# Optimization experiments

Measured on AMD Instinct MI355X. Metric: run time of the kernel, lower is better.

## Reference

```python
import jax, jax.numpy as jnp
import numpy as np

B, N, K = 2, 8192, 9
FEAT_C, COST_C, FLOW_C = 128, 64, 3
CH = [128, 128]          # PointConv output channels
MLP = [128, 64]          # pointwise Conv1d channels
WN = 16                  # WeightNet output width
HID = [8, 8]             # WeightNet hidden widths
SLOPE = 0.1              # leaky relu slope
EPS = 1e-5
CLAMP = (-200.0, 200.0)


def setup_inputs() -> dict:
    key = jax.random.key(0)
    ks = iter(jax.random.split(key, 64))
    def nrm(shape, s=0.02):
        return jax.random.normal(next(ks), shape, jnp.float32) * s
    inp = {}
    inp["xyz"] = jax.random.normal(next(ks), (B, N, 3), jnp.float32)
    inp["feats"] = jax.random.normal(next(ks), (B, FEAT_C, N), jnp.float32)
    inp["cost_volume"] = jax.random.normal(next(ks), (B, COST_C, N), jnp.float32)
    inp["flow"] = jax.random.normal(next(ks), (B, FLOW_C, N), jnp.float32)
    last = FEAT_C + COST_C + FLOW_C
    for i, co in enumerate(CH):
        cin = last + 3
        p = f"pc{i}_"
        inp[p + "w1"] = nrm((HID[0], 3)); inp[p + "b1"] = jnp.zeros((HID[0],), jnp.float32)
        inp[p + "w2"] = nrm((HID[1], HID[0])); inp[p + "b2"] = jnp.zeros((HID[1],), jnp.float32)
        inp[p + "w3"] = nrm((WN, HID[1])); inp[p + "b3"] = jnp.zeros((WN,), jnp.float32)
        inp[p + "linW"] = nrm((co, cin * WN)); inp[p + "linb"] = jnp.zeros((co,), jnp.float32)
        last = co
    for i, co in enumerate(MLP):
        inp[f"mlp{i}_W"] = nrm((co, last)); inp[f"mlp{i}_b"] = jnp.zeros((co,), jnp.float32)
        last = co
    inp["fc_W"] = nrm((3, last)); inp["fc_b"] = jnp.zeros((3,), jnp.float32)
    return inp


def _bn(x, axes):
    m = x.mean(axes, keepdims=True)
    v = x.var(axes, keepdims=True)
    return (x - m) / jnp.sqrt(v + EPS)


def _leaky(x):
    return jnp.where(x >= 0, x, SLOPE * x)


def _knn_idx(xyz, k):
    # xyz: [B,N,3] -> idx [B,N,K] of k nearest (incl. self)
    sq = jnp.sum(xyz * xyz, -1)                       # [B,N]
    d = sq[:, :, None] + sq[:, None, :] - 2.0 * jnp.einsum('bnc,bmc->bnm', xyz, xyz)
    return jax.lax.top_k(-d, k)[1]                    # [B,N,K]


def _gather(a, idx):
    # a: [B,N,C], idx: [B,N,K] -> [B,N,K,C]
    return jax.vmap(lambda x, i: x[i])(a, idx)


def _pointconv(xyz, points, idx, w1, b1, w2, b2, w3, b3, linW, linb):
    # xyz [B,N,3], points [B,C,N] -> [B,out,N]
    g_xyz = _gather(xyz, idx) - xyz[:, :, None, :]    # [B,N,K,3] relative coords
    g_pts = _gather(jnp.transpose(points, (0, 2, 1)), idx)  # [B,N,K,C]
    grouped = jnp.concatenate([g_pts, g_xyz], -1)     # [B,N,K,C+3]
    # WeightNet on relative coords: 3 -> 8 -> 8 -> 16 (bn+relu each)
    h = jax.nn.relu(_bn(g_xyz @ w1.T + b1, (0, 1, 2)))
    h = jax.nn.relu(_bn(h @ w2.T + b2, (0, 1, 2)))
    w = jax.nn.relu(_bn(h @ w3.T + b3, (0, 1, 2)))    # [B,N,K,WN]
    bsz, n = grouped.shape[0], grouped.shape[1]
    agg = jnp.einsum('bnkc,bnkw->bncw', grouped, w).reshape(bsz, n, -1)
    out = agg @ linW.T + linb                         # [B,N,out]
    out = _leaky(_bn(out, (0, 1)))
    return jnp.transpose(out, (0, 2, 1))              # [B,out,N]


def reference(xyz, feats, cost_volume, flow,
              pc0_w1, pc0_b1, pc0_w2, pc0_b2, pc0_w3, pc0_b3, pc0_linW, pc0_linb,
              pc1_w1, pc1_b1, pc1_w2, pc1_b2, pc1_w3, pc1_b3, pc1_linW, pc1_linb,
              mlp0_W, mlp0_b, mlp1_W, mlp1_b, fc_W, fc_b):
    idx = _knn_idx(xyz, K)
    x = jnp.concatenate([feats, cost_volume, flow], axis=1)  # [B, feat+cost+flow, N]
    x = _pointconv(xyz, x, idx, pc0_w1, pc0_b1, pc0_w2, pc0_b2, pc0_w3, pc0_b3, pc0_linW, pc0_linb)
    x = _pointconv(xyz, x, idx, pc1_w1, pc1_b1, pc1_w2, pc1_b2, pc1_w3, pc1_b3, pc1_linW, pc1_linb)
    x = _leaky(jnp.einsum('oc,bcn->bon', mlp0_W, x) + mlp0_b[None, :, None])
    x = _leaky(jnp.einsum('oc,bcn->bon', mlp1_W, x) + mlp1_b[None, :, None])
    fl = jnp.einsum('oc,bcn->bon', fc_W, x) + fc_b[None, :, None]
    return x, jnp.clip(fl, CLAMP[0], CLAMP[1])
```

## Files before the change

### kernel.cpp

```cpp
#include <hip/hip_runtime.h>

#define NBATCH 2
#define NPTS   8192
#define NPT    (NBATCH*NPTS)
#define KNN    9
#define SEG    16
#define SEGN   (NPTS/SEG)
#define SCAP   16
#define SSTR   17

typedef unsigned short u16;
typedef unsigned int   u32;
typedef short bf16x8 __attribute__((ext_vector_type(8)));
typedef float f32x4  __attribute__((ext_vector_type(4)));

__device__ __forceinline__ float wred(float v){
#pragma unroll
  for(int o=32;o>0;o>>=1) v += __shfl_down(v,o);
  return v;
}

__device__ __forceinline__ u16 f2b(float f){
  u32 u = __float_as_uint(f);
  return (u16)((u + 0x7fffu + ((u>>16)&1u)) >> 16);
}

__device__ __forceinline__ float bumpup(float x){
  u32 u = __float_as_uint(x);
  if(u == 0x80000000u) u = 1u;
  else if((int)u >= 0) u += 1u;
  else u -= 1u;
  return __uint_as_float(u);
}

__global__ __launch_bounds__(256) void k_build_xin(
    const float* __restrict__ feats, const float* __restrict__ cost,
    const float* __restrict__ flow, float* __restrict__ xin)
{
  __shared__ float buf[196][67];
  int t = threadIdx.x;
  int pt0 = blockIdx.x*64;
  int b = pt0 >> 13, n0 = pt0 & (NPTS-1);
  int lane = t & 63, grp = t >> 6;
  const float* f  = feats + (size_t)b*128*NPTS + n0 + lane;
  const float* cv = cost  + (size_t)b*64 *NPTS + n0 + lane;
  const float* fl = flow  + (size_t)b*3  *NPTS + n0 + lane;
  for(int c=grp; c<128; c+=4) buf[c][lane]      = f[(size_t)c*NPTS];
  for(int c=grp; c<64;  c+=4) buf[128+c][lane]  = cv[(size_t)c*NPTS];
  if(grp<3) buf[192+grp][lane] = fl[(size_t)grp*NPTS];
  else      buf[195][lane] = 0.f;
  __syncthreads();
  for(int e=t; e<64*49; e+=256){
    int p = e/49, q = e-p*49;
    float4 v = make_float4(buf[4*q][p], buf[4*q+1][p], buf[4*q+2][p], buf[4*q+3][p]);
    *(float4*)(xin + (size_t)(pt0+p)*196 + 4*q) = v;
  }
}

__global__ __launch_bounds__(256) void k_xyzs(
    const float* __restrict__ xyz, float4* __restrict__ xs)
{
  int pt = blockIdx.x*256 + threadIdx.x;
  int b = pt >> 13, n = pt & (NPTS-1);
  const float* p = xyz + (size_t)b*NPTS*3 + 3*n;
  float x=p[0], y=p[1], z=p[2];
  float s = __fadd_rn(__fadd_rn(__fmul_rn(x,x),__fmul_rn(y,y)),__fmul_rn(z,z));
  xs[pt] = make_float4(x,y,z,s);
}

__global__ __launch_bounds__(256) void k_thr(
    const float4* __restrict__ xs, float* __restrict__ thr)
{
  __shared__ float md[4][64][9];
  int t = threadIdx.x, lane = t & 63, wave = t >> 6;
  int qb = blockIdx.x;
  int b = qb >> 7;
  int n = (qb & 127)*64 + lane;
  const float4* xb4 = xs + (size_t)b*NPTS;
  float4 q = xb4[n];
  float qx=q.x, qy=q.y, qz=q.z, qs=q.w;
  float bd[KNN];
#pragma unroll
  for(int i=0;i<KNN;i++) bd[i]=__builtin_inff();
  for(int i=0;i<128;i++){
    int m = (wave*128 + i)*16;
    float4 c = xb4[m];
    float dot = fmaf(c.z,qz, fmaf(c.y,qy, __fmul_rn(c.x,qx)));
    float d = __fsub_rn(__fadd_rn(qs,c.w), __fmul_rn(2.0f,dot));
    if(d < bd[KNN-1]){
      bd[KNN-1]=d;
#pragma unroll
      for(int r=KNN-2;r>=0;r--){
        if(bd[r+1] < bd[r]){ float td=bd[r]; bd[r]=bd[r+1]; bd[r+1]=td; }
      }
    }
  }
#pragma unroll
  for(int i=0;i<KNN;i++) md[wave][lane][i]=bd[i];
  __syncthreads();
  if(t < 64){
    float b2[KNN];
#pragma unroll
    for(int i=0;i<KNN;i++) b2[i]=__builtin_inff();
    for(int w=0;w<4;w++){
#pragma unroll
      for(int i=0;i<KNN;i++){
        float d = md[w][t][i];
        if(d < b2[KNN-1]){
          b2[KNN-1]=d;
#pragma unroll
          for(int r=KNN-2;r>=0;r--){
            if(b2[r+1] < b2[r]){ float td=b2[r]; b2[r]=b2[r+1]; b2[r+1]=td; }
          }
        }
      }
    }
    thr[(b<<13) + (qb & 127)*64 + t] = b2[KNN-1];
  }
}

__global__ __launch_bounds__(256) void k_knn_part(
    const float4* __restrict__ xs, const float* __restrict__ thr,
    float* __restrict__ pd, int* __restrict__ pi)
{
  __shared__ float sdq[256*SSTR];
  __shared__ int   sqi[256*SSTR];
  int t = threadIdx.x;
  int seg = blockIdx.x & (SEG-1);
  int qc  = blockIdx.x >> 4;
  int b = qc >> 5;
  int n = (qc & 31)*256 + t;
  int pt = (b<<13) + n;
  const float4* xb4 = xs + (size_t)b*NPTS;
  float4 q = xb4[n];
  float qx=q.x, qy=q.y, qz=q.z, qs=q.w;
  float init = bumpup(thr[pt]);
  float bd[KNN]; int bi[KNN];
#pragma unroll
  for(int i=0;i<KNN;i++){ bd[i]=init; bi[i]=0x7fffffff; }
  float cut = init;
  int cnt = 0;
  float* msd = sdq + t*SSTR;
  int*   msi = sqi + t*SSTR;
  auto flush = [&](){
    for(int i=0;i<cnt;i++){
      float d = msd[i]; int id = msi[i];
      if(d < bd[KNN-1]){
        bd[KNN-1]=d; bi[KNN-1]=id;
#pragma unroll
        for(int r=KNN-2;r>=0;r--){
          if(bd[r+1] < bd[r]){
            float td=bd[r]; bd[r]=bd[r+1]; bd[r+1]=td;
            int ti=bi[r]; bi[r]=bi[r+1]; bi[r+1]=ti;
          }
        }
      }
    }
    cnt = 0;
    cut = bd[KNN-1];
  };
  const int m0 = seg*SEGN;
  for(int j0=0; j0<SEGN; j0+=8){
    float dv[8];
#pragma unroll
    for(int u=0;u<8;u++){
      float4 c = xb4[m0+j0+u];
      float dot = fmaf(c.z,qz, fmaf(c.y,qy, __fmul_rn(c.x,qx)));
      dv[u] = __fsub_rn(__fadd_rn(qs,c.w), __fmul_rn(2.0f,dot));
    }
#pragma unroll
    for(int u=0;u<8;u++){
      if(dv[u] < cut){
        msd[cnt]=dv[u]; msi[cnt]=m0+j0+u; cnt++;
        if(cnt==SCAP) flush();
      }
    }
  }
  flush();
  size_t base = ((size_t)pt*SEG + seg)*KNN;
#pragma unroll
  for(int i=0;i<KNN;i++){ pd[base+i]=bd[i]; pi[base+i]=bi[i]; }
}

__global__ __launch_bounds__(256) void k_knn_merge(
    const float* __restrict__ xyz,
    const float* __restrict__ pd, const int* __restrict__ pi,
    int* __restrict__ idxo, float* __restrict__ gpart)
{
  __shared__ float red[4][9];
  int t = threadIdx.x;
  int pt = blockIdx.x*256 + t;
  int b = pt >> 13, n = pt & (NPTS-1);
  const float* xb = xyz + (size_t)b*NPTS*3;
  const float4* dp = (const float4*)(pd + (size_t)pt*SEG*KNN);
  const int4*   ip = (const int4*)(pi + (size_t)pt*SEG*KNN);
  float bd[KNN]; int bi[KNN];
#pragma unroll
  for(int i=0;i<KNN;i++){ bd[i]=__builtin_inff(); bi[i]=0x7fffffff; }
  for(int v=0; v<SEG*KNN/4; v++){
    float4 dv = dp[v];
    int4   iv = ip[v];
    float dd[4] = {dv.x,dv.y,dv.z,dv.w};
    int   ii[4] = {iv.x,iv.y,iv.z,iv.w};
#pragma unroll
    for(int u=0;u<4;u++){
      float d = dd[u]; int id = ii[u];
      if(d < bd[KNN-1]){
        bd[KNN-1]=d; bi[KNN-1]=id;
#pragma unroll
        for(int i=KNN-2;i>=0;i--){
          if(bd[i+1] < bd[i]){
            float td=bd[i]; bd[i]=bd[i+1]; bd[i+1]=td;
            int ti=bi[i]; bi[i]=bi[i+1]; bi[i+1]=ti;
          }
        }
      }
    }
  }
#pragma unroll
  for(int r=0;r<KNN;r++) idxo[pt*KNN + r] = bi[r];
  float q0=xb[3*n], q1=xb[3*n+1], q2=xb[3*n+2];
  float mom[9];
#pragma unroll
  for(int i=0;i<9;i++) mom[i]=0.f;
#pragma unroll
  for(int r=0;r<KNN;r++){
    int m = bi[r];
    float gx=xb[3*m]-q0, gy=xb[3*m+1]-q1, gz=xb[3*m+2]-q2;
    mom[0]+=gx; mom[1]+=gy; mom[2]+=gz;
    mom[3]=fmaf(gx,gx,mom[3]); mom[4]=fmaf(gy,gy,mom[4]); mom[5]=fmaf(gz,gz,mom[5]);
    mom[6]=fmaf(gx,gy,mom[6]); mom[7]=fmaf(gx,gz,mom[7]); mom[8]=fmaf(gy,gz,mom[8]);
  }
  int wave = t>>6, lane = t&63;
#pragma unroll
  for(int i=0;i<9;i++){
    float s = wred(mom[i]);
    if(lane==0) red[wave][i]=s;
  }
  __syncthreads();
  if(t<9)
    gpart[blockIdx.x*9 + t] = red[0][t]+red[1][t]+red[2][t]+red[3][t];
}

__global__ __launch_bounds__(256) void k_wn23a2(
    const float* __restrict__ xyz, const int* __restrict__ idx,
    const float* __restrict__ gpart, float cnt,
    const float* __restrict__ W1a, const float* __restrict__ B1a,
    const float* __restrict__ W2a, const float* __restrict__ B2a,
    const float* __restrict__ W1b, const float* __restrict__ B1b,
    const float* __restrict__ W2b, const float* __restrict__ B2b,
    float* __restrict__ houta, float* __restrict__ houtb,
    float* __restrict__ parta, float* __restrict__ partb)
{
  __shared__ float mom[9];
  __shared__ float stl[2][16];
  __shared__ float red[4][2][8];
  int t = threadIdx.x;
  if(t<9){
    float s=0.f;
    for(int r=0;r<64;r++) s += gpart[r*9+t];
    mom[t]=s;
  }
  __syncthreads();
  if(t<16){
    int L = t>>3, j = t&7;
    const float* W1 = L? W1b : W1a;
    const float* B1 = L? B1b : B1a;
    float inv = 1.0f/cnt;
    float w0=W1[3*j], w1=W1[3*j+1], w2=W1[3*j+2], bb=B1[j];
    float Eg0=mom[0]*inv, Eg1=mom[1]*inv, Eg2=mom[2]*inv;
    float Mxx=mom[3]*inv, Myy=mom[4]*inv, Mzz=mom[5]*inv;
    float Mxy=mom[6]*inv, Mxz=mom[7]*inv, Myz=mom[8]*inv;
    float mu_lin = w0*Eg0 + w1*Eg1 + w2*Eg2;
    float mean = mu_lin + bb;
    float e2 = w0*w0*Mxx + w1*w1*Myy + w2*w2*Mzz
             + 2.f*(w0*w1*Mxy + w0*w2*Mxz + w1*w2*Myz)
             + 2.f*bb*mu_lin + bb*bb;
    float var = e2 - mean*mean;
    stl[L][j] = mean;
    stl[L][8+j] = 1.0f/sqrtf(var + 1e-5f);
  }
  __syncthreads();
  int e = blockIdx.x*256 + t;
  int pt = e/KNN;
  int b = pt>>13, n = pt & (NPTS-1);
  int m = idx[e];
  const float* xb = xyz + (size_t)b*NPTS*3;
  float gx = xb[3*m]-xb[3*n], gy = xb[3*m+1]-xb[3*n+1], gz = xb[3*m+2]-xb[3*n+2];
  int wave = t>>6, lane = t&63;
#pragma unroll
  for(int L=0; L<2; L++){
    const float* W1 = L? W1b : W1a;
    const float* B1 = L? B1b : B1a;
    const float* W2 = L? W2b : W2a;
    const float* B2 = L? B2b : B2a;
    float* hout = L? houtb : houta;
    float* part = L? partb : parta;
    float x[8];
#pragma unroll
    for(int j=0;j<8;j++){
      float d = fmaf(gz, W1[3*j+2], fmaf(gy, W1[3*j+1], gx*W1[3*j]));
      float v = d + B1[j];
      v = (v - stl[L][j])*stl[L][8+j];
      x[j] = v>0.f? v : 0.f;
    }
    float v[8];
#pragma unroll
    for(int j=0;j<8;j++){
      float d = 0.f;
#pragma unroll
      for(int i=0;i<8;i++) d = fmaf(x[i], W2[j*8+i], d);
      v[j] = d + B2[j];
      hout[(size_t)e*8 + j] = v[j];
    }
#pragma unroll
    for(int j=0;j<8;j++){
      float s = wred(v[j]);
      float q = wred(v[j]*v[j]);
      if(lane==0){ red[wave][0][j]=s; red[wave][1][j]=q; }
    }
    __syncthreads();
    if(t < 16){
      int isq = t>>3, c = t&7;
      part[blockIdx.x*16 + t] =
        red[0][isq][c]+red[1][isq][c]+red[2][isq][c]+red[3][isq][c];
    }
    __syncthreads();
  }
}

__global__ __launch_bounds__(256) void k_wn23_2(
    const float* __restrict__ hina, const float* __restrict__ pina,
    const float* __restrict__ hinb, const float* __restrict__ pinb,
    int nb, float cnt,
    const float* __restrict__ Wa, const float* __restrict__ Ba,
    const float* __restrict__ Wb, const float* __restrict__ Bb,
    float* __restrict__ houta, float* __restrict__ houtb,
    float* __restrict__ parta, float* __restrict__ partb)
{
  __shared__ float sa[256], qa[256];
  __shared__ float stl[16];
  __shared__ float red[4][2][16];
  int t = threadIdx.x;
  int e = blockIdx.x*256 + t;
  int wave = t>>6, lane = t&63;
#pragma unroll
  for(int L=0; L<2; L++){
    const float* hin = L? hinb : hina;
    const float* pin = L? pinb : pina;
    const float* W   = L? Wb : Wa;
    const float* Bv  = L? Bb : Ba;
    float* hout = L? houtb : houta;
    float* part = L? partb : parta;
    {
      int c = t % 8;
      int r0 = t / 8;
      float s=0.f, q=0.f;
      for(int r=r0; r<nb; r+=32){
        s += pin[r*16 + c];
        q += pin[r*16 + 8 + c];
      }
      sa[t]=s; qa[t]=q;
      __syncthreads();
      if(t < 8){
        for(int g=1; g<32; g++){ s += sa[t+g*8]; q += qa[t+g*8]; }
        float mean = s/cnt;
        float var  = q/cnt - mean*mean;
        stl[t]   = mean;
        stl[8+t] = 1.0f/sqrtf(var + 1e-5f);
      }
      __syncthreads();
    }
    float x[8];
#pragma unroll
    for(int i=0;i<8;i++){
      float v = (hin[(size_t)e*8 + i] - stl[i])*stl[8+i];
      x[i] = v>0.f? v : 0.f;
    }
    float v[16];
#pragma unroll
    for(int j=0;j<16;j++){
      float d = 0.f;
#pragma unroll
      for(int i=0;i<8;i++) d = fmaf(x[i], W[j*8+i], d);
      v[j] = d + Bv[j];
      hout[(size_t)e*16 + j] = v[j];
    }
#pragma unroll
    for(int j=0;j<16;j++){
      float s = wred(v[j]);
      float q = wred(v[j]*v[j]);
      if(lane==0){ red[wave][0][j]=s; red[wave][1][j]=q; }
    }
    __syncthreads();
    if(t < 32){
      int isq = t>>4, c = t&15;
      part[blockIdx.x*32 + t] =
        red[0][isq][c]+red[1][isq][c]+red[2][isq][c]+red[3][isq][c];
    }
    __syncthreads();
  }
}

__global__ __launch_bounds__(256) void k_fin2(
    const float* __restrict__ pa, const float* __restrict__ pb,
    float* __restrict__ sta, float* __restrict__ stb, int nb, float cnt)
{
  __shared__ float sa[256], qa[256];
  int t = threadIdx.x;
  const int C = 16;
#pragma unroll
  for(int L=0; L<2; L++){
    const float* partial = L? pb : pa;
    float* st = L? stb : sta;
    int c = t % C;
    int r0 = t / C;
    int stride = 256 / C;
    float s=0.f, q=0.f;
    for(int r=r0; r<nb; r+=stride){
      s += partial[r*2*C + c];
      q += partial[r*2*C + C + c];
    }
    sa[t]=s; qa[t]=q;
    __syncthreads();
    if(t < C){
      for(int g=1; g<stride; g++){ s += sa[t+g*C]; q += qa[t+g*C]; }
      float mean = s/cnt;
      float var  = q/cnt - mean*mean;
      st[t]   = mean;
      st[C+t] = 1.0f/sqrtf(var + 1e-5f);
    }
    __syncthreads();
  }
}

__global__ __launch_bounds__(256) void k_fin(
    const float* __restrict__ partial, float* __restrict__ st,
    int C, int nb, float cnt)
{
  __shared__ float sa[256], qa[256];
  int t = threadIdx.x;
  int c = t % C;
  int r0 = t / C;
  int stride = 256 / C;
  float s=0.f, q=0.f;
  for(int r=r0; r<nb; r+=stride){
    s += partial[r*2*C + c];
    q += partial[r*2*C + C + c];
  }
  sa[t]=s; qa[t]=q;
  __syncthreads();
  if(t < C){
    for(int g=1; g<stride; g++){ s += sa[t+g*C]; q += qa[t+g*C]; }
    float mean = s/cnt;
    float var  = q/cnt - mean*mean;
    st[t]   = mean;
    st[C+t] = 1.0f/sqrtf(var + 1e-5f);
  }
}

__global__ __launch_bounds__(256) void k_prepW(
    const float* __restrict__ linW, u16* __restrict__ Wh, int AW, int KP)
{
  int e = blockIdx.x*256 + threadIdx.x;
  if(e >= 128*KP) return;
  int o = e / KP, k = e - o*KP;
  float w = (k < AW) ? linW[o*AW + k] : 0.f;
  Wh[e] = f2b(w);
}

template<int CIN, int XSTRIDE, int KP, bool BN>
__global__ __launch_bounds__(256) void k_buildA(
    const float* __restrict__ xin, const float* __restrict__ xyz,
    const int* __restrict__ idx, const float* __restrict__ wpre,
    const float* __restrict__ st3, const float* __restrict__ bnst,
    u16* __restrict__ Abuf, int c0)
{
  constexpr int P = 16;
  constexpr int CPTS = CIN-3;
  constexpr int CPAD = KP/16;
  __shared__ float wm[P][KNN][16];
  __shared__ float gxs[P][KNN][3];
  __shared__ int   si[P][KNN];
  __shared__ float sm3[16], sr3[16];
  int t = threadIdx.x;
  int pt0 = c0 + blockIdx.x*P;
  int b = pt0 >> 13;
  const float* xb = xyz + (size_t)b*NPTS*3;
  if(t<16){ sm3[t]=st3[t]; sr3[t]=st3[16+t]; }
  for(int e=t; e<P*KNN; e+=256){
    int p = e/KNN, k = e - p*KNN;
    int n = (pt0+p)&(NPTS-1);
    int m = idx[(pt0+p)*KNN+k];
    si[p][k]=m;
    gxs[p][k][0]=xb[3*m]  -xb[3*n];
    gxs[p][k][1]=xb[3*m+1]-xb[3*n+1];
    gxs[p][k][2]=xb[3*m+2]-xb[3*n+2];
  }
  __syncthreads();
  for(int e=t; e<P*KNN*16; e+=256){
    int p = e/(KNN*16); int r = e - p*(KNN*16); int k = r>>4, wn = r&15;
    float v = (wpre[((size_t)(pt0+p)*KNN + k)*16 + wn] - sm3[wn]) * sr3[wn];
    wm[p][k][wn] = v>0.f? v:0.f;
  }
  __syncthreads();
  for(int it=t; it<P*CPAD; it+=256){
    int p = it/CPAD, c = it - p*CPAD;
    u32 u[8];
    if(c < CIN){
      float g[KNN];
      if(c < CPTS){
#pragma unroll
        for(int k=0;k<KNN;k++)
          g[k] = xin[(size_t)((b<<13) + si[p][k])*XSTRIDE + c];
        if(BN){
          float sm = bnst[c], sr = bnst[128+c];
#pragma unroll
          for(int k=0;k<KNN;k++){
            float v = (g[k]-sm)*sr;
            g[k] = v>=0.f? v : 0.1f*v;
          }
        }
      } else {
        int cc = c - CPTS;
#pragma unroll
        for(int k=0;k<KNN;k++) g[k] = gxs[p][k][cc];
      }
      float a[16];
#pragma unroll
      for(int wn=0; wn<16; wn++){
        float s = 0.f;
#pragma unroll
        for(int k=0;k<KNN;k++) s = fmaf(g[k], wm[p][k][wn], s);
        a[wn] = s;
      }
#pragma unroll
      for(int j=0;j<8;j++)
        u[j] = (u32)f2b(a[2*j]) | ((u32)f2b(a[2*j+1])<<16);
    } else {
#pragma unroll
      for(int j=0;j<8;j++) u[j]=0;
    }
    u32* dst = (u32*)(Abuf + ((size_t)(blockIdx.x*P + p)*KP + c*16));
    *(uint4*)dst       = make_uint4(u[0],u[1],u[2],u[3]);
    *((uint4*)dst + 1) = make_uint4(u[4],u[5],u[6],u[7]);
  }
}

__device__ __forceinline__ void gload16(const void* g, void* l){
  __builtin_amdgcn_global_load_lds(
      (const __attribute__((address_space(1))) u32*)g,
      (__attribute__((address_space(3))) u32*)l, 16, 0, 0);
}

template<int KP>
__global__ __launch_bounds__(512) void k_gemm(
    const u16* __restrict__ Wh, const u16* __restrict__ A,
    const float* __restrict__ linb, float* __restrict__ outp,
    float* __restrict__ partial, int ptBase)
{
  __shared__ __attribute__((aligned(16))) u16 lds[24576];
  constexpr int NT = KP/64;
  int t = threadIdx.x, wave = t>>6, lane = t&63;
  int p0 = blockIdx.x*64;
  const u16* Ab = A + (size_t)p0*KP;

  auto stage = [&](const u16* __restrict__ g, int k0, int ldsByteOff, int rows){
    int nr = (rows*128) >> 13;
    for(int r=0;r<nr;r++){
      int y  = (r*8 + wave) << 10;
      int yl = y + lane*16;
      int row = yl >> 7;
      int s = (yl >> 4) & 7;
      int c = s ^ (row & 7);
      const u16* src = g + (size_t)row*KP + k0 + c*8;
      gload16(src, (char*)lds + ldsByteOff + y);
    }
  };

  stage(Wh, 0, 0,     128);
  stage(Ab, 0, 32768, 64);

  f32x4 acc[4];
#pragma unroll
  for(int j=0;j<4;j++) acc[j]=(f32x4)(0.f);

  for(int kt=0; kt<NT; kt++){
    int cur = kt & 1;
    __syncthreads();
    if(kt+1 < NT){
      int nxt = cur^1;
      stage(Wh, (kt+1)*64, nxt*16384,         128);
      stage(Ab, (kt+1)*64, 32768 + nxt*8192,  64);
    }
    const u16* Lw = lds + cur*8192;
    const u16* La = lds + 16384 + cur*4096;
#pragma unroll
    for(int kf=0; kf<2; kf++){
      int cb = kf*4 + (lane>>4);
      bf16x8 af[4];
#pragma unroll
      for(int nf=0; nf<4; nf++){
        int p = nf*16 + (lane&15);
        af[nf] = *(const bf16x8*)(La + p*64 + ((cb ^ (p&7))<<3));
      }
      int row = wave*16 + (lane&15);
      bf16x8 wh = *(const bf16x8*)(Lw + row*64 + ((cb ^ (row&7))<<3));
#pragma unroll
      for(int nf=0; nf<4; nf++)
        acc[nf] = __builtin_amdgcn_mfma_f32_16x16x32_bf16(wh, af[nf], acc[nf], 0,0,0);
    }
  }

  int gb = (ptBase>>6) + blockIdx.x;
  int q = lane>>4, lc = lane&15;
  int obase = wave*16 + q*4;
#pragma unroll
  for(int r=0;r<4;r++){
    int o = obase + r;
    float bo = linb[o];
    float sv = 0.f, qv = 0.f;
#pragma unroll
    for(int nf=0; nf<4; nf++){
      float x = acc[nf][r] + bo;
      outp[(size_t)(ptBase + p0 + nf*16 + lc)*128 + o] = x;
      sv += x; qv = fmaf(x,x,qv);
    }
#pragma unroll
    for(int off=8; off>0; off>>=1){
      sv += __shfl_down(sv,off);
      qv += __shfl_down(qv,off);
    }
    if(lc==0){
      partial[gb*256 + o]       = sv;
      partial[gb*256 + 128 + o] = qv;
    }
  }
}

__global__ __launch_bounds__(512) void k_mlp(
    const float* __restrict__ outp1, const float* __restrict__ sto,
    const float* __restrict__ W0, const float* __restrict__ B0,
    const float* __restrict__ W1, const float* __restrict__ B1,
    const float* __restrict__ Wf, const float* __restrict__ Bf,
    float* __restrict__ dout)
{
  __shared__ float w0l[128*129];
  __shared__ float w1l[128*65];
  __shared__ float xt [128*65];
  __shared__ float m1l[64*65];
  int t = threadIdx.x;
  int pt0 = blockIdx.x*64;
  int b = pt0 >> 13, n0 = pt0 & (NPTS-1);
  for(int e=t; e<128*128; e+=512){ int o=e>>7, j=e&127; w0l[j*129+o] = W0[e]; }
  for(int e=t; e<64*128;  e+=512){ int o=e>>7, j=e&127; w1l[j*65+o]  = W1[e]; }
  for(int e=t; e<64*128;  e+=512){
    int p=e>>7, j=e&127;
    float v = outp1[(size_t)(pt0+p)*128 + j];
    v = (v - sto[j])*sto[128+j];
    xt[j*65+p] = v>=0.f? v : 0.1f*v;
  }
  __syncthreads();
  int p = t&63, wv = t>>6;
  float acc[16];
#pragma unroll
  for(int i=0;i<16;i++) acc[i]=0.f;
  for(int j=0;j<128;j++){
    float xv = xt[j*65+p];
#pragma unroll
    for(int i=0;i<16;i++)
      acc[i] = fmaf(w0l[j*129 + wv*16 + i], xv, acc[i]);
  }
  __syncthreads();
#pragma unroll
  for(int i=0;i<16;i++){
    int o = wv*16+i;
    float v = acc[i] + B0[o];
    v = v>=0.f? v : 0.1f*v;
    xt[o*65 + p] = v;
  }
  __syncthreads();
  float a2[8];
#pragma unroll
  for(int i=0;i<8;i++) a2[i]=0.f;
  for(int j=0;j<128;j++){
    float xv = xt[j*65+p];
#pragma unroll
    for(int i=0;i<8;i++)
      a2[i] = fmaf(w1l[j*65 + wv*8 + i], xv, a2[i]);
  }
#pragma unroll
  for(int i=0;i<8;i++){
    int o = wv*8+i;
    float v = a2[i] + B1[o];
    v = v>=0.f? v : 0.1f*v;
    dout[(size_t)(b*64+o)*NPTS + n0 + p] = v;
    m1l[o*65+p] = v;
  }
  __syncthreads();
  if(t < 192){
    int o = t/64, pp = t%64;
    float a = Bf[o];
    for(int j=0;j<64;j++) a = fmaf(Wf[o*64+j], m1l[j*65+pp], a);
    a = fminf(fmaxf(a, -200.f), 200.f);
    dout[(size_t)NBATCH*64*NPTS + (size_t)(b*3+o)*NPTS + n0 + pp] = a;
  }
}

extern "C" void kernel_launch(void* const* d_in, const int* in_sizes, int n_in,
                              void* d_out, int out_size, void* d_ws, size_t ws_size,
                              hipStream_t stream)
{
  (void)in_sizes; (void)n_in; (void)out_size;
  const float* xyz   = (const float*)d_in[0];
  const float* feats = (const float*)d_in[1];
  const float* cost  = (const float*)d_in[2];
  const float* flow  = (const float*)d_in[3];
  const float* pw1[2]  = {(const float*)d_in[4],  (const float*)d_in[12]};
  const float* pb1[2]  = {(const float*)d_in[5],  (const float*)d_in[13]};
  const float* pw2[2]  = {(const float*)d_in[6],  (const float*)d_in[14]};
  const float* pb2[2]  = {(const float*)d_in[7],  (const float*)d_in[15]};
  const float* pw3[2]  = {(const float*)d_in[8],  (const float*)d_in[16]};
  const float* pb3[2]  = {(const float*)d_in[9],  (const float*)d_in[17]};
  const float* plW[2]  = {(const float*)d_in[10], (const float*)d_in[18]};
  const float* plb[2]  = {(const float*)d_in[11], (const float*)d_in[19]};
  const float* m0W = (const float*)d_in[20];
  const float* m0b = (const float*)d_in[21];
  const float* m1W = (const float*)d_in[22];
  const float* m1b = (const float*)d_in[23];
  const float* fcW = (const float*)d_in[24];
  const float* fcb = (const float*)d_in[25];
  float* out = (float*)d_out;

  const int KP0 = 3200, AW0 = 3168;
  const int KP1 = 2112, AW1 = 2096;

  float* ws = (float*)d_ws;
  size_t o = 0;
  float* xin0 = ws + o; o += (size_t)NPT*196;
  int*   idx  = (int*)(ws + o); o += (size_t)NPT*KNN + 3;
  o &= ~(size_t)3;
  float4* xs  = (float4*)(ws + o); o += (size_t)NPT*4;
  float* thr  = ws + o; o += (size_t)NPT;
  float* pd   = ws + o; o += (size_t)NPT*SEG*KNN;
  int*   pi   = (int*)(ws + o); o += (size_t)NPT*SEG*KNN;
  float* h2a  = ws + o; o += (size_t)NPT*KNN*8;
  float* h2b  = ws + o; o += (size_t)NPT*KNN*8;
  float* wpre0 = ws + o; o += (size_t)NPT*KNN*16;
  float* wpre1 = ws + o; o += (size_t)NPT*KNN*16;
  float* gpart = ws + o; o += 64*9 + 7;
  float* part2a = ws + o; o += 576*16;
  float* part2b = ws + o; o += 576*16;
  float* part3a = ws + o; o += 576*32;
  float* part3b = ws + o; o += 576*32;
  float* parto = ws + o; o += 65536;
  float* st3a = ws + o; o += 32;
  float* st3b = ws + o; o += 32;
  float* sto0 = ws + o; o += 256;
  float* sto1 = ws + o; o += 256;
  float* outp0 = ws + o; o += (size_t)NPT*128;
  float* outp1 = ws + o; o += (size_t)NPT*128;
  u16* Wh0 = (u16*)(ws + o); o += (size_t)128*KP0/2;
  u16* Wh1 = (u16*)(ws + o); o += (size_t)128*KP1/2;
  u16* Abuf = (u16*)(ws + o);
  size_t used_bytes = o*4;
  size_t avail = ws_size > used_bytes ? ws_size - used_bytes : 0;
  int npc = NPT;
  while(npc > 1024 && (size_t)npc*KP0*2 > avail) npc >>= 1;

  k_build_xin<<<NPT/64, 256, 0, stream>>>(feats, cost, flow, xin0);
  k_xyzs<<<NPT/256, 256, 0, stream>>>(xyz, xs);
  k_thr<<<256, 256, 0, stream>>>(xs, thr);
  k_knn_part<<<64*SEG, 256, 0, stream>>>(xs, thr, pd, pi);
  k_knn_merge<<<NPT/256, 256, 0, stream>>>(xyz, pd, pi, idx, gpart);

  k_prepW<<<(128*KP0+255)/256, 256, 0, stream>>>(plW[0], Wh0, AW0, KP0);
  k_prepW<<<(128*KP1+255)/256, 256, 0, stream>>>(plW[1], Wh1, AW1, KP1);

  const float cnt1 = (float)(NPT*KNN);
  const float cnto = (float)NPT;

  k_wn23a2<<<576,256,0,stream>>>(xyz, idx, gpart, cnt1,
                                 pw1[0], pb1[0], pw2[0], pb2[0],
                                 pw1[1], pb1[1], pw2[1], pb2[1],
                                 h2a, h2b, part2a, part2b);
  k_wn23_2<<<576,256,0,stream>>>(h2a, part2a, h2b, part2b, 576, cnt1,
                                 pw3[0], pb3[0], pw3[1], pb3[1],
                                 wpre0, wpre1, part3a, part3b);
  k_fin2<<<1,256,0,stream>>>(part3a, part3b, st3a, st3b, 576, cnt1);

  for(int c0 = 0; c0 < NPT; c0 += npc){
    k_buildA<198,196,KP0,false><<<npc/16,256,0,stream>>>(xin0, xyz, idx, wpre0, st3a, sto0, Abuf, c0);
    k_gemm<KP0><<<npc/64,512,0,stream>>>(Wh0, Abuf, plb[0], outp0, parto, c0);
  }
  k_fin<<<1,256,0,stream>>>(parto, sto0, 128, NPT/64, cnto);

  for(int c0 = 0; c0 < NPT; c0 += npc){
    k_buildA<131,128,KP1,true><<<npc/16,256,0,stream>>>(outp0, xyz, idx, wpre1, st3b, sto0, Abuf, c0);
    k_gemm<KP1><<<npc/64,512,0,stream>>>(Wh1, Abuf, plb[1], outp1, parto, c0);
  }
  k_fin<<<1,256,0,stream>>>(parto, sto1, 128, NPT/64, cnto);

  k_mlp<<<NPT/64,512,0,stream>>>(outp1, sto1, m0W,m0b, m1W,m1b, fcW,fcb, out);
}
```

Before: 543.1 us.

## Fuse xyz prep and weight prep, drop stored kNN distances, double segments

The xyz/squared-norm packing is folded into the feature transpose kernel, and the two weight-conversion launches are merged into one, removing launches. The kNN partial stage now stores only candidate indices and recomputes distances from the packed coordinates during flushes and in the merge, so the partial-distance buffer and its traffic go away. The segment count doubles to 32 with a smaller candidate stash, which raises parallelism in the partial search but doubles the merge work and adds gather loads for recomputation.

```diff
diff --git a/kernel.cpp b/kernel.cpp
--- a/kernel.cpp
+++ b/kernel.cpp
@@ -4,10 +4,10 @@
 #define NPTS   8192
 #define NPT    (NBATCH*NPTS)
 #define KNN    9
-#define SEG    16
+#define SEG    32
 #define SEGN   (NPTS/SEG)
-#define SCAP   16
-#define SSTR   17
+#define SCAP   8
+#define SSTR   9
 
 typedef unsigned short u16;
 typedef unsigned int   u32;
@@ -35,7 +35,8 @@
 
 __global__ __launch_bounds__(256) void k_build_xin(
     const float* __restrict__ feats, const float* __restrict__ cost,
-    const float* __restrict__ flow, float* __restrict__ xin)
+    const float* __restrict__ flow, const float* __restrict__ xyz,
+    float* __restrict__ xin, float4* __restrict__ xs)
 {
   __shared__ float buf[196][67];
   int t = threadIdx.x;
@@ -49,23 +50,19 @@
   for(int c=grp; c<64;  c+=4) buf[128+c][lane]  = cv[(size_t)c*NPTS];
   if(grp<3) buf[192+grp][lane] = fl[(size_t)grp*NPTS];
   else      buf[195][lane] = 0.f;
+  if(t < 64){
+    int pt = pt0 + t;
+    const float* p = xyz + (size_t)b*NPTS*3 + 3*(pt & (NPTS-1));
+    float x=p[0], y=p[1], z=p[2];
+    float s = __fadd_rn(__fadd_rn(__fmul_rn(x,x),__fmul_rn(y,y)),__fmul_rn(z,z));
+    xs[pt] = make_float4(x,y,z,s);
+  }
   __syncthreads();
   for(int e=t; e<64*49; e+=256){
     int p = e/49, q = e-p*49;
     float4 v = make_float4(buf[4*q][p], buf[4*q+1][p], buf[4*q+2][p], buf[4*q+3][p]);
     *(float4*)(xin + (size_t)(pt0+p)*196 + 4*q) = v;
   }
-}
-
-__global__ __launch_bounds__(256) void k_xyzs(
-    const float* __restrict__ xyz, float4* __restrict__ xs)
-{
-  int pt = blockIdx.x*256 + threadIdx.x;
-  int b = pt >> 13, n = pt & (NPTS-1);
-  const float* p = xyz + (size_t)b*NPTS*3 + 3*n;
-  float x=p[0], y=p[1], z=p[2];
-  float s = __fadd_rn(__fadd_rn(__fmul_rn(x,x),__fmul_rn(y,y)),__fmul_rn(z,z));
-  xs[pt] = make_float4(x,y,z,s);
 }
 
 __global__ __launch_bounds__(256) void k_thr(
@@ -121,13 +118,12 @@
 
 __global__ __launch_bounds__(256) void k_knn_part(
     const float4* __restrict__ xs, const float* __restrict__ thr,
-    float* __restrict__ pd, int* __restrict__ pi)
-{
-  __shared__ float sdq[256*SSTR];
-  __shared__ int   sqi[256*SSTR];
+    int* __restrict__ pi)
+{
+  __shared__ int sqi[256*SSTR];
   int t = threadIdx.x;
   int seg = blockIdx.x & (SEG-1);
-  int qc  = blockIdx.x >> 4;
+  int qc  = blockIdx.x >> 5;
   int b = qc >> 5;
   int n = (qc & 31)*256 + t;
   int pt = (b<<13) + n;
@@ -140,11 +136,13 @@
   for(int i=0;i<KNN;i++){ bd[i]=init; bi[i]=0x7fffffff; }
   float cut = init;
   int cnt = 0;
-  float* msd = sdq + t*SSTR;
-  int*   msi = sqi + t*SSTR;
+  int* msi = sqi + t*SSTR;
   auto flush = [&](){
     for(int i=0;i<cnt;i++){
-      float d = msd[i]; int id = msi[i];
+      int id = msi[i];
+      float4 c = xb4[id];
+      float dot = fmaf(c.z,qz, fmaf(c.y,qy, __fmul_rn(c.x,qx)));
+      float d = __fsub_rn(__fadd_rn(qs,c.w), __fmul_rn(2.0f,dot));
       if(d < bd[KNN-1]){
         bd[KNN-1]=d; bi[KNN-1]=id;
 #pragma unroll
@@ -171,7 +169,7 @@
 #pragma unroll
     for(int u=0;u<8;u++){
       if(dv[u] < cut){
-        msd[cnt]=dv[u]; msi[cnt]=m0+j0+u; cnt++;
+        msi[cnt] = m0+j0+u; cnt++;
         if(cnt==SCAP) flush();
       }
     }
@@ -179,39 +177,42 @@
   flush();
   size_t base = ((size_t)pt*SEG + seg)*KNN;
 #pragma unroll
-  for(int i=0;i<KNN;i++){ pd[base+i]=bd[i]; pi[base+i]=bi[i]; }
+  for(int i=0;i<KNN;i++) pi[base+i]=bi[i];
 }
 
 __global__ __launch_bounds__(256) void k_knn_merge(
-    const float* __restrict__ xyz,
-    const float* __restrict__ pd, const int* __restrict__ pi,
+    const float4* __restrict__ xs, const int* __restrict__ pi,
     int* __restrict__ idxo, float* __restrict__ gpart)
 {
   __shared__ float red[4][9];
   int t = threadIdx.x;
   int pt = blockIdx.x*256 + t;
-  int b = pt >> 13, n = pt & (NPTS-1);
-  const float* xb = xyz + (size_t)b*NPTS*3;
-  const float4* dp = (const float4*)(pd + (size_t)pt*SEG*KNN);
-  const int4*   ip = (const int4*)(pi + (size_t)pt*SEG*KNN);
+  int b = pt >> 13;
+  const float4* xb4 = xs + (size_t)b*NPTS;
+  float4 q = xb4[pt & (NPTS-1)];
+  float qx=q.x, qy=q.y, qz=q.z, qs=q.w;
+  const int4* ip = (const int4*)(pi + (size_t)pt*SEG*KNN);
   float bd[KNN]; int bi[KNN];
 #pragma unroll
   for(int i=0;i<KNN;i++){ bd[i]=__builtin_inff(); bi[i]=0x7fffffff; }
   for(int v=0; v<SEG*KNN/4; v++){
-    float4 dv = dp[v];
-    int4   iv = ip[v];
-    float dd[4] = {dv.x,dv.y,dv.z,dv.w};
-    int   ii[4] = {iv.x,iv.y,iv.z,iv.w};
+    int4 iv = ip[v];
+    int ii[4] = {iv.x,iv.y,iv.z,iv.w};
 #pragma unroll
     for(int u=0;u<4;u++){
-      float d = dd[u]; int id = ii[u];
-      if(d < bd[KNN-1]){
-        bd[KNN-1]=d; bi[KNN-1]=id;
-#pragma unroll
-        for(int i=KNN-2;i>=0;i--){
-          if(bd[i+1] < bd[i]){
-            float td=bd[i]; bd[i]=bd[i+1]; bd[i+1]=td;
-            int ti=bi[i]; bi[i]=bi[i+1]; bi[i+1]=ti;
+      int id = ii[u];
+      if(id != 0x7fffffff){
+        float4 c = xb4[id];
+        float dot = fmaf(c.z,qz, fmaf(c.y,qy, __fmul_rn(c.x,qx)));
+        float d = __fsub_rn(__fadd_rn(qs,c.w), __fmul_rn(2.0f,dot));
+        if(d < bd[KNN-1]){
+          bd[KNN-1]=d; bi[KNN-1]=id;
+#pragma unroll
+          for(int i=KNN-2;i>=0;i--){
+            if(bd[i+1] < bd[i]){
+              float td=bd[i]; bd[i]=bd[i+1]; bd[i+1]=td;
+              int ti=bi[i]; bi[i]=bi[i+1]; bi[i+1]=ti;
+            }
           }
         }
       }
@@ -219,14 +220,14 @@
   }
 #pragma unroll
   for(int r=0;r<KNN;r++) idxo[pt*KNN + r] = bi[r];
-  float q0=xb[3*n], q1=xb[3*n+1], q2=xb[3*n+2];
   float mom[9];
 #pragma unroll
   for(int i=0;i<9;i++) mom[i]=0.f;
 #pragma unroll
   for(int r=0;r<KNN;r++){
     int m = bi[r];
-    float gx=xb[3*m]-q0, gy=xb[3*m+1]-q1, gz=xb[3*m+2]-q2;
+    float4 c = xb4[m];
+    float gx=c.x-qx, gy=c.y-qy, gz=c.z-qz;
     mom[0]+=gx; mom[1]+=gy; mom[2]+=gz;
     mom[3]=fmaf(gx,gx,mom[3]); mom[4]=fmaf(gy,gy,mom[4]); mom[5]=fmaf(gz,gz,mom[5]);
     mom[6]=fmaf(gx,gy,mom[6]); mom[7]=fmaf(gx,gz,mom[7]); mom[8]=fmaf(gy,gz,mom[8]);
@@ -459,14 +460,23 @@
   }
 }
 
-__global__ __launch_bounds__(256) void k_prepW(
-    const float* __restrict__ linW, u16* __restrict__ Wh, int AW, int KP)
+__global__ __launch_bounds__(256) void k_prepW2(
+    const float* __restrict__ W0, u16* __restrict__ Wh0,
+    const float* __restrict__ W1, u16* __restrict__ Wh1)
 {
   int e = blockIdx.x*256 + threadIdx.x;
-  if(e >= 128*KP) return;
-  int o = e / KP, k = e - o*KP;
-  float w = (k < AW) ? linW[o*AW + k] : 0.f;
-  Wh[e] = f2b(w);
+  const int N0 = 128*3200;
+  if(e < N0){
+    int o = e / 3200, k = e - o*3200;
+    float w = (k < 3168) ? W0[o*3168 + k] : 0.f;
+    Wh0[e] = f2b(w);
+  } else {
+    int e1 = e - N0;
+    if(e1 >= 128*2112) return;
+    int o = e1 / 2112, k = e1 - o*2112;
+    float w = (k < 2096) ? W1[o*2096 + k] : 0.f;
+    Wh1[e1] = f2b(w);
+  }
 }
 
 template<int CIN, int XSTRIDE, int KP, bool BN>
@@ -732,8 +742,8 @@
   const float* fcb = (const float*)d_in[25];
   float* out = (float*)d_out;
 
-  const int KP0 = 3200, AW0 = 3168;
-  const int KP1 = 2112, AW1 = 2096;
+  const int KP0 = 3200;
+  const int KP1 = 2112;
 
   float* ws = (float*)d_ws;
   size_t o = 0;
@@ -742,7 +752,6 @@
   o &= ~(size_t)3;
   float4* xs  = (float4*)(ws + o); o += (size_t)NPT*4;
   float* thr  = ws + o; o += (size_t)NPT;
-  float* pd   = ws + o; o += (size_t)NPT*SEG*KNN;
   int*   pi   = (int*)(ws + o); o += (size_t)NPT*SEG*KNN;
   float* h2a  = ws + o; o += (size_t)NPT*KNN*8;
   float* h2b  = ws + o; o += (size_t)NPT*KNN*8;
@@ -768,14 +777,12 @@
   int npc = NPT;
   while(npc > 1024 && (size_t)npc*KP0*2 > avail) npc >>= 1;
 
-  k_build_xin<<<NPT/64, 256, 0, stream>>>(feats, cost, flow, xin0);
-  k_xyzs<<<NPT/256, 256, 0, stream>>>(xyz, xs);
+  k_build_xin<<<NPT/64, 256, 0, stream>>>(feats, cost, flow, xyz, xin0, xs);
   k_thr<<<256, 256, 0, stream>>>(xs, thr);
-  k_knn_part<<<64*SEG, 256, 0, stream>>>(xs, thr, pd, pi);
-  k_knn_merge<<<NPT/256, 256, 0, stream>>>(xyz, pd, pi, idx, gpart);
-
-  k_prepW<<<(128*KP0+255)/256, 256, 0, stream>>>(plW[0], Wh0, AW0, KP0);
-  k_prepW<<<(128*KP1+255)/256, 256, 0, stream>>>(plW[1], Wh1, AW1, KP1);
+  k_knn_part<<<64*SEG, 256, 0, stream>>>(xs, thr, pi);
+  k_knn_merge<<<NPT/256, 256, 0, stream>>>(xs, pi, idx, gpart);
+
+  k_prepW2<<<(128*(KP0+KP1)+255)/256, 256, 0, stream>>>(plW[0], Wh0, plW[1], Wh1);
 
   const float cnt1 = (float)(NPT*KNN);
   const float cnto = (float)NPT;
```

Measured after the change: 580.1 us. +6.8%, slower.
